# Kernel optimization log

Measured on AMD Instinct MI355X. Metric: run time of the kernel, lower is better.

Reference implementation:

```python
import jax, jax.numpy as jnp
import numpy as np

N = 100000
EPS = 1e-16

def gat_conv(x, edge_index, W, a_src, a_dst, bias, heads, out_c):
    # x: [N, F_in]; W: [F_in, heads*out_c]; a_src/a_dst: [heads, out_c]; bias: [heads*out_c]
    n = x.shape[0]
    loops = jnp.arange(n)
    src = jnp.concatenate([edge_index[0], loops])  # add self loops (PyG default)
    dst = jnp.concatenate([edge_index[1], loops])
    h = (x @ W).reshape(n, heads, out_c)                       # [N,H,C]
    s_src = jnp.sum(h * a_src[None], axis=-1)                  # [N,H]
    s_dst = jnp.sum(h * a_dst[None], axis=-1)                  # [N,H]
    e = jax.nn.leaky_relu(s_src[src] + s_dst[dst], 0.2)        # [E,H]
    m = jax.ops.segment_max(e, dst, num_segments=n)            # [N,H]
    ex = jnp.exp(e - m[dst])
    denom = jax.ops.segment_sum(ex, dst, num_segments=n)       # [N,H]
    alpha = ex / (denom[dst] + EPS)                            # [E,H]
    msg = h[src] * alpha[:, :, None]                           # [E,H,C]
    out = jax.ops.segment_sum(msg, dst, num_segments=n)        # [N,H,C]
    return out.reshape(n, heads * out_c) + bias

def setup_inputs() -> dict:
    key = jax.random.key(0)
    ks = jax.random.split(key, 10)
    num_features, num_classes, H = 512, 10, 8
    E = 3200000
    x = jax.random.normal(ks[0], (N, num_features), dtype=jnp.float32)
    edge_index = jax.random.randint(ks[1], (2, E), 0, N, dtype=jnp.int64)
    g = lambda k, shape, fan: jax.random.normal(k, shape, dtype=jnp.float32) * (1.0 / np.sqrt(fan))
    W1 = g(ks[2], (num_features, H * 8), num_features)
    a_src1 = g(ks[3], (H, 8), 8)
    a_dst1 = g(ks[4], (H, 8), 8)
    b1 = jnp.zeros((H * 8,), dtype=jnp.float32)
    W2 = g(ks[5], (H * 8, H * num_classes), H * 8)
    a_src2 = g(ks[6], (H, num_classes), num_classes)
    a_dst2 = g(ks[7], (H, num_classes), num_classes)
    b2 = jnp.zeros((H * num_classes,), dtype=jnp.float32)
    return {"x": x, "edge_index": edge_index, "W1": W1, "a_src1": a_src1,
            "a_dst1": a_dst1, "b1": b1, "W2": W2, "a_src2": a_src2,
            "a_dst2": a_dst2, "b2": b2}

def reference(x, edge_index, W1, a_src1, a_dst1, b1, W2, a_src2, a_dst2, b2):
    # inference mode: dropout = identity
    h = jax.nn.elu(gat_conv(x, edge_index, W1, a_src1, a_dst1, b1, heads=8, out_c=8))
    out = gat_conv(h, edge_index, W2, a_src2, a_dst2, b2, heads=8, out_c=10)
    return jax.nn.log_softmax(out, axis=1)
```

## Files before the change

### kernel.cpp

```cpp
#include <hip/hip_runtime.h>
#include <math.h>

#define NN 100000
#define NE 3200000
#define FIN 512
#define NH 8
#define C1 8
#define HC1 64
#define C2 10
#define HC2 80

#define EPB 4096
#define NBLK 782
#define NBUK 196
#define SCN (NBUK * NBLK)
#define SCNB 150

typedef unsigned int uint;
typedef unsigned short ushort;
using bf16x8 = __attribute__((ext_vector_type(8))) short;
using f32x4  = __attribute__((ext_vector_type(4))) float;

__device__ float g_h1[NN * HC1];
__device__ float g_hact[NN * HC1];
__device__ float g_h2[NN * HC2];
__device__ uint  g_h1b[NN * 32];
__device__ uint  g_h2b[NN * 40];
__device__ uint  g_w1bt[64 * 256];
__device__ float g_ssrc[NN * NH];
__device__ float g_sdst[NN * NH];
__device__ int   g_off[NN + 1];
__device__ uint  g_pscan[SCN];
__device__ uint  g_bsum2[256];
__device__ uint  g_ebuf[NE];
__device__ int   g_csr[NE];

__device__ __forceinline__ float lrelu(float x) { return fmaxf(x, 0.2f * x); }

__device__ __forceinline__ uint bf16_rne(float x) {
  uint u = __float_as_uint(x);
  u += 0x7fffu + ((u >> 16) & 1u);
  return u >> 16;
}
__device__ __forceinline__ uint packbf2(float lo, float hi) {
  return bf16_rne(lo) | (bf16_rne(hi) << 16);
}
__device__ __forceinline__ float blo(uint v) { return __uint_as_float(v << 16); }
__device__ __forceinline__ float bhi(uint v) { return __uint_as_float(v & 0xffff0000u); }

__global__ __launch_bounds__(256) void p1count_kernel(const int* __restrict__ ei) {
  __shared__ uint cnt[NBUK];
  int tid = threadIdx.x;
  for (int i = tid; i < NBUK; i += 256) cnt[i] = 0;
  __syncthreads();
  const int* dstp = ei + NE;
  int base = blockIdx.x * EPB;
#pragma unroll 4
  for (int k = 0; k < 16; k++) {
    int e = base + k * 256 + tid;
    if (e < NE) atomicAdd(&cnt[dstp[e] >> 9], 1u);
  }
  __syncthreads();
  for (int i = tid; i < NBUK; i += 256) g_pscan[i * NBLK + blockIdx.x] = cnt[i];
}

__global__ __launch_bounds__(1024) void scn_block_kernel() {
  __shared__ uint sd[1024];
  int tid = threadIdx.x;
  int i = blockIdx.x * 1024 + tid;
  uint v = (i < SCN) ? g_pscan[i] : 0;
  sd[tid] = v;
  __syncthreads();
  for (int off = 1; off < 1024; off <<= 1) {
    uint x = (tid >= off) ? sd[tid - off] : 0;
    __syncthreads();
    sd[tid] += x;
    __syncthreads();
  }
  if (i < SCN) g_pscan[i] = sd[tid] - v;
  if (tid == 1023) g_bsum2[blockIdx.x] = sd[1023];
}

__global__ void scn_tops_kernel() {
  __shared__ uint sd[256];
  int tid = threadIdx.x;
  uint v = (tid < SCNB) ? g_bsum2[tid] : 0;
  sd[tid] = v;
  __syncthreads();
  for (int off = 1; off < 256; off <<= 1) {
    uint x = (tid >= off) ? sd[tid - off] : 0;
    __syncthreads();
    sd[tid] += x;
    __syncthreads();
  }
  g_bsum2[tid] = sd[tid] - v;
}

__global__ __launch_bounds__(1024) void scn_add_kernel() {
  int i = blockIdx.x * 1024 + threadIdx.x;
  if (i < SCN) g_pscan[i] += g_bsum2[i >> 10];
}

__global__ __launch_bounds__(256) void p1scatter_kernel(const int* __restrict__ ei) {
  __shared__ uint cur[NBUK];
  int tid = threadIdx.x;
  for (int i = tid; i < NBUK; i += 256) cur[i] = g_pscan[i * NBLK + blockIdx.x];
  __syncthreads();
  const int* srcp = ei;
  const int* dstp = ei + NE;
  int base = blockIdx.x * EPB;
#pragma unroll 4
  for (int k = 0; k < 16; k++) {
    int e = base + k * 256 + tid;
    if (e < NE) {
      int d = dstp[e], s = srcp[e];
      uint pos = atomicAdd(&cur[d >> 9], 1u);
      g_ebuf[pos] = ((uint)(d & 511) << 17) | (uint)s;
    }
  }
}

__global__ __launch_bounds__(1024) void p2build_kernel() {
  __shared__ uint hist[4096];
  __shared__ uint excl[4096];
  __shared__ uint tsum[1024];
  int tid = threadIdx.x;
  int b = blockIdx.x;
  uint bstart = g_pscan[b * NBLK];
  uint bend = (b < NBUK - 1) ? g_pscan[(b + 1) * NBLK] : NE;
  for (int i = tid; i < 4096; i += 1024) hist[i] = 0;
  __syncthreads();
  for (uint j = bstart + tid; j < bend; j += 1024) {
    uint v = g_ebuf[j];
    uint bin = ((v >> 17) << 3) | ((v & 0x1FFFFu) >> 14);
    atomicAdd(&hist[bin], 1u);
  }
  __syncthreads();
  uint h0 = hist[tid * 4 + 0], h1 = hist[tid * 4 + 1];
  uint h2 = hist[tid * 4 + 2], h3 = hist[tid * 4 + 3];
  uint s1 = h0 + h1, s2 = s1 + h2, s3 = s2 + h3;
  tsum[tid] = s3;
  __syncthreads();
  for (int off = 1; off < 1024; off <<= 1) {
    uint x = (tid >= off) ? tsum[tid - off] : 0;
    __syncthreads();
    tsum[tid] += x;
    __syncthreads();
  }
  uint te = tsum[tid] - s3;
  excl[tid * 4 + 0] = te;
  excl[tid * 4 + 1] = te + h0;
  excl[tid * 4 + 2] = te + s1;
  excl[tid * 4 + 3] = te + s2;
  __syncthreads();
  if (tid < 512) {
    int dst = b * 512 + tid;
    if (dst < NN) g_off[dst] = (int)(bstart + excl[tid * 8]);
  }
  if (b == NBUK - 1 && tid == 0) g_off[NN] = NE;
  for (int i = tid; i < 4096; i += 1024) hist[i] = excl[i];
  __syncthreads();
  for (uint j = bstart + tid; j < bend; j += 1024) {
    uint v = g_ebuf[j];
    uint bin = ((v >> 17) << 3) | ((v & 0x1FFFFu) >> 14);
    uint pos = bstart + atomicAdd(&hist[bin], 1u);
    g_csr[pos] = (int)(v & 0x1FFFFu);
  }
}

__global__ __launch_bounds__(256) void w1cast_kernel(const float* __restrict__ W) {
  int idx = blockIdx.x * 256 + threadIdx.x;
  int n = idx & 63, kp = idx >> 6;
  float lo = W[(2 * kp) * HC1 + n];
  float hi = W[(2 * kp + 1) * HC1 + n];
  g_w1bt[n * 256 + kp] = packbf2(lo, hi);
}

__device__ __forceinline__ int sw_idx(int row, int g) {
  return row * 32 + ((g ^ (row & 7)) << 2);
}

__global__ __launch_bounds__(256) void gemm1_kernel(const float* __restrict__ X) {
  __shared__ uint sA[64 * 32];
  __shared__ uint sB[64 * 32];
  int t = threadIdx.x;
  int w = t >> 6, l = t & 63;
  int q = l >> 4, c = l & 15;
  int r0 = blockIdx.x * 64;
  int sr = t >> 2;
  int sc = t & 3;
  int xrow = r0 + sr; if (xrow >= NN) xrow = NN - 1;
  const float* xbase = &X[(long)xrow * FIN + sc * 16];
  const uint* wbase = &g_w1bt[sr * 256 + sc * 8];
  f32x4 acc[4] = {{0.f,0.f,0.f,0.f},{0.f,0.f,0.f,0.f},{0.f,0.f,0.f,0.f},{0.f,0.f,0.f,0.f}};
  for (int k0 = 0; k0 < FIN; k0 += 64) {
    __syncthreads();
    float4 f0 = *(const float4*)&xbase[k0 + 0];
    float4 f1 = *(const float4*)&xbase[k0 + 4];
    float4 f2 = *(const float4*)&xbase[k0 + 8];
    float4 f3 = *(const float4*)&xbase[k0 + 12];
    uint4 a0 = make_uint4(packbf2(f0.x, f0.y), packbf2(f0.z, f0.w),
                          packbf2(f1.x, f1.y), packbf2(f1.z, f1.w));
    uint4 a1 = make_uint4(packbf2(f2.x, f2.y), packbf2(f2.z, f2.w),
                          packbf2(f3.x, f3.y), packbf2(f3.z, f3.w));
    *(uint4*)&sA[sw_idx(sr, sc * 2 + 0)] = a0;
    *(uint4*)&sA[sw_idx(sr, sc * 2 + 1)] = a1;
    uint4 b0 = *(const uint4*)&wbase[(k0 >> 1) + 0];
    uint4 b1 = *(const uint4*)&wbase[(k0 >> 1) + 4];
    *(uint4*)&sB[sw_idx(sr, sc * 2 + 0)] = b0;
    *(uint4*)&sB[sw_idx(sr, sc * 2 + 1)] = b1;
    __syncthreads();
#pragma unroll
    for (int ks = 0; ks < 2; ks++) {
      int g = ks * 4 + q;
      bf16x8 a = *(const bf16x8*)&sA[sw_idx(w * 16 + c, g)];
#pragma unroll
      for (int nt = 0; nt < 4; nt++) {
        bf16x8 b = *(const bf16x8*)&sB[sw_idx(nt * 16 + c, g)];
        acc[nt] = __builtin_amdgcn_mfma_f32_16x16x32_bf16(a, b, acc[nt], 0, 0, 0);
      }
    }
  }
  int orow0 = r0 + w * 16 + q * 4;
#pragma unroll
  for (int nt = 0; nt < 4; nt++) {
#pragma unroll
    for (int r = 0; r < 4; r++) {
      int row = orow0 + r;
      if (row < NN) g_h1[row * HC1 + nt * 16 + c] = acc[nt][r];
    }
  }
}

template <int LAYER>
__global__ __launch_bounds__(256) void s_kernel(const float* __restrict__ a_src,
                                                const float* __restrict__ a_dst) {
  constexpr int C = (LAYER == 1) ? C1 : C2;
  const float* Hm = (LAYER == 1) ? g_h1 : g_h2;
  uint* Hb = (LAYER == 1) ? g_h1b : g_h2b;
  int t = blockIdx.x * 256 + threadIdx.x;
  if (t >= NN * NH) return;
  int h = t & 7;
  const float* row = &Hm[t * C];
  float ss = 0.f, sdd = 0.f;
  float vals[C];
#pragma unroll
  for (int c = 0; c < C; c++) {
    float v = row[c];
    vals[c] = v;
    ss = fmaf(v, a_src[h * C + c], ss);
    sdd = fmaf(v, a_dst[h * C + c], sdd);
  }
  g_ssrc[t] = ss;
  g_sdst[t] = sdd;
#pragma unroll
  for (int j = 0; j < C / 2; j++)
    Hb[t * (C / 2) + j] = packbf2(vals[2 * j], vals[2 * j + 1]);
}

__global__ __launch_bounds__(256) void agg1_kernel(const float* __restrict__ b1) {
  int gw = __builtin_amdgcn_readfirstlane((int)((blockIdx.x * 256 + threadIdx.x) >> 6));
  if (gw >= NN) return;
  int lane = threadIdx.x & 63;
  int h = lane >> 3;
  const ushort* __restrict__ h1u = (const ushort*)g_h1b;
  float sd = g_sdst[gw * NH + h];
  int begin = g_off[gw];
  int cnt = g_off[gw + 1] - begin;
  float acc = 0.f, wsum = 0.f;
  int j = 0;
  for (; j + 4 <= cnt; j += 4) {
    int s0 = __builtin_amdgcn_readfirstlane(g_csr[begin + j + 0]);
    int s1 = __builtin_amdgcn_readfirstlane(g_csr[begin + j + 1]);
    int s2 = __builtin_amdgcn_readfirstlane(g_csr[begin + j + 2]);
    int s3 = __builtin_amdgcn_readfirstlane(g_csr[begin + j + 3]);
    float t0 = g_ssrc[s0 * NH + h];
    float t1 = g_ssrc[s1 * NH + h];
    float t2 = g_ssrc[s2 * NH + h];
    float t3 = g_ssrc[s3 * NH + h];
    uint v0 = h1u[s0 * HC1 + lane];
    uint v1 = h1u[s1 * HC1 + lane];
    uint v2 = h1u[s2 * HC1 + lane];
    uint v3 = h1u[s3 * HC1 + lane];
    float e0 = __expf(lrelu(t0 + sd));
    float e1 = __expf(lrelu(t1 + sd));
    float e2 = __expf(lrelu(t2 + sd));
    float e3 = __expf(lrelu(t3 + sd));
    acc = fmaf(__uint_as_float(v0 << 16), e0, acc);
    acc = fmaf(__uint_as_float(v1 << 16), e1, acc);
    acc = fmaf(__uint_as_float(v2 << 16), e2, acc);
    acc = fmaf(__uint_as_float(v3 << 16), e3, acc);
    wsum += (e0 + e1) + (e2 + e3);
  }
  for (; j < cnt; j++) {
    int s = __builtin_amdgcn_readfirstlane(g_csr[begin + j]);
    float e = __expf(lrelu(g_ssrc[s * NH + h] + sd));
    acc = fmaf(__uint_as_float((uint)h1u[s * HC1 + lane] << 16), e, acc);
    wsum += e;
  }
  float es = __expf(lrelu(g_ssrc[gw * NH + h] + sd));
  acc = fmaf(g_h1[gw * HC1 + lane], es, acc);
  wsum += es;
  float v = acc * (1.f / wsum) + b1[lane];
  g_hact[gw * HC1 + lane] = v > 0.f ? v : __expf(v) - 1.f;
}

__global__ __launch_bounds__(256) void gemm2_kernel(const float* __restrict__ W) {
  __shared__ float sW[64 * HC2 + 64];
  int tid = threadIdx.x;
  for (int i = tid; i < 64 * HC2; i += 256) sW[i] = W[i];
  for (int i = 64 * HC2 + tid; i < 64 * HC2 + 64; i += 256) sW[i] = 0.f;
  __syncthreads();
  int lane = tid & 63;
  int w0 = (blockIdx.x * 256 + tid) >> 6;
  for (int r = w0; r < NN; r += 8192) {
    float v = g_hact[r * HC1 + lane];
    float acc0 = 0.f, acc1 = 0.f;
#pragma unroll
    for (int k = 0; k < 64; k++) {
      float xk = __shfl(v, k);
      acc0 = fmaf(xk, sW[k * HC2 + lane], acc0);
      acc1 = fmaf(xk, sW[k * HC2 + 64 + lane], acc1);
    }
    g_h2[r * HC2 + lane] = acc0;
    if (lane < 16) g_h2[r * HC2 + 64 + lane] = acc1;
  }
}

__global__ __launch_bounds__(256) void agg2_kernel(float* __restrict__ out,
                                                   const float* __restrict__ b2) {
  int gw = __builtin_amdgcn_readfirstlane((int)((blockIdx.x * 256 + threadIdx.x) >> 6));
  if (gw >= NN) return;
  int lane = threadIdx.x & 63;
  int p = lane < 40 ? lane : 39;
  int h = p / 5;
  float sd = g_sdst[gw * NH + h];
  int begin = g_off[gw];
  int cnt = g_off[gw + 1] - begin;
  float acc0 = 0.f, acc1 = 0.f, wsum = 0.f;
  int j = 0;
  for (; j + 4 <= cnt; j += 4) {
    int s0 = __builtin_amdgcn_readfirstlane(g_csr[begin + j + 0]);
    int s1 = __builtin_amdgcn_readfirstlane(g_csr[begin + j + 1]);
    int s2 = __builtin_amdgcn_readfirstlane(g_csr[begin + j + 2]);
    int s3 = __builtin_amdgcn_readfirstlane(g_csr[begin + j + 3]);
    float t0 = g_ssrc[s0 * NH + h];
    float t1 = g_ssrc[s1 * NH + h];
    float t2 = g_ssrc[s2 * NH + h];
    float t3 = g_ssrc[s3 * NH + h];
    uint v0 = g_h2b[s0 * 40 + p];
    uint v1 = g_h2b[s1 * 40 + p];
    uint v2 = g_h2b[s2 * 40 + p];
    uint v3 = g_h2b[s3 * 40 + p];
    float e0 = __expf(lrelu(t0 + sd));
    float e1 = __expf(lrelu(t1 + sd));
    float e2 = __expf(lrelu(t2 + sd));
    float e3 = __expf(lrelu(t3 + sd));
    acc0 = fmaf(blo(v0), e0, acc0); acc1 = fmaf(bhi(v0), e0, acc1);
    acc0 = fmaf(blo(v1), e1, acc0); acc1 = fmaf(bhi(v1), e1, acc1);
    acc0 = fmaf(blo(v2), e2, acc0); acc1 = fmaf(bhi(v2), e2, acc1);
    acc0 = fmaf(blo(v3), e3, acc0); acc1 = fmaf(bhi(v3), e3, acc1);
    wsum += (e0 + e1) + (e2 + e3);
  }
  for (; j < cnt; j++) {
    int s = __builtin_amdgcn_readfirstlane(g_csr[begin + j]);
    float e = __expf(lrelu(g_ssrc[s * NH + h] + sd));
    uint v = g_h2b[s * 40 + p];
    acc0 = fmaf(blo(v), e, acc0); acc1 = fmaf(bhi(v), e, acc1);
    wsum += e;
  }
  float es = __expf(lrelu(g_ssrc[gw * NH + h] + sd));
  acc0 = fmaf(g_h2[gw * HC2 + 2 * p], es, acc0);
  acc1 = fmaf(g_h2[gw * HC2 + 2 * p + 1], es, acc1);
  wsum += es;
  float inv = 1.f / wsum;
  float v0 = acc0 * inv + b2[2 * p];
  float v1 = acc1 * inv + b2[2 * p + 1];
  float mx = fmaxf(v0, v1);
  for (int o = 32; o; o >>= 1) mx = fmaxf(mx, __shfl_xor(mx, o));
  float spart = (lane < 40) ? __expf(v0 - mx) + __expf(v1 - mx) : 0.f;
  for (int o = 32; o; o >>= 1) spart += __shfl_xor(spart, o);
  float lse = mx + __logf(spart);
  if (lane < 40) *(float2*)&out[gw * HC2 + 2 * p] = make_float2(v0 - lse, v1 - lse);
}

extern "C" void kernel_launch(void* const* d_in, const int* in_sizes, int n_in,
                              void* d_out, int out_size, void* d_ws, size_t ws_size,
                              hipStream_t stream) {
  (void)in_sizes; (void)n_in; (void)out_size; (void)d_ws; (void)ws_size;
  const float* x   = (const float*)d_in[0];
  const int*   ei  = (const int*)d_in[1];
  const float* W1  = (const float*)d_in[2];
  const float* as1 = (const float*)d_in[3];
  const float* ad1 = (const float*)d_in[4];
  const float* b1  = (const float*)d_in[5];
  const float* W2  = (const float*)d_in[6];
  const float* as2 = (const float*)d_in[7];
  const float* ad2 = (const float*)d_in[8];
  const float* b2  = (const float*)d_in[9];
  float* out = (float*)d_out;

  p1count_kernel<<<NBLK, 256, 0, stream>>>(ei);
  scn_block_kernel<<<SCNB, 1024, 0, stream>>>();
  scn_tops_kernel<<<1, 256, 0, stream>>>();
  scn_add_kernel<<<SCNB, 1024, 0, stream>>>();
  p1scatter_kernel<<<NBLK, 256, 0, stream>>>(ei);
  p2build_kernel<<<NBUK, 1024, 0, stream>>>();

  w1cast_kernel<<<64, 256, 0, stream>>>(W1);
  gemm1_kernel<<<1563, 256, 0, stream>>>(x);
  s_kernel<1><<<3125, 256, 0, stream>>>(as1, ad1);
  agg1_kernel<<<25000, 256, 0, stream>>>(b1);

  gemm2_kernel<<<2048, 256, 0, stream>>>(W2);
  s_kernel<2><<<3125, 256, 0, stream>>>(as2, ad2);
  agg2_kernel<<<25000, 256, 0, stream>>>(out, b2);
}
```

Before: 794.4 us.

## Aggregate eight nodes per wave in source-range rounds for cache locality

The CSR build now keeps per-node offsets split into eight source-index sub-ranges (g_off8). Each aggregation wave handles eight destination nodes and walks the sub-ranges in rounds, starting at a different round per block (blockIdx & 7) and placing a block-wide barrier after each round. The aim is for concurrently running waves to gather from the same slice of source features at once, so the random gathers hit in L2/MALL instead of DRAM. In exchange it launches fewer waves, holds more per-wave registers, and adds barriers and extra offset loads.

```diff
diff --git a/kernel.cpp b/kernel.cpp
--- a/kernel.cpp
+++ b/kernel.cpp
@@ -29,7 +29,7 @@
 __device__ uint  g_w1bt[64 * 256];
 __device__ float g_ssrc[NN * NH];
 __device__ float g_sdst[NN * NH];
-__device__ int   g_off[NN + 1];
+__device__ int   g_off8[NBUK * 4096];
 __device__ uint  g_pscan[SCN];
 __device__ uint  g_bsum2[256];
 __device__ uint  g_ebuf[NE];
@@ -153,11 +153,8 @@
   excl[tid * 4 + 2] = te + s1;
   excl[tid * 4 + 3] = te + s2;
   __syncthreads();
-  if (tid < 512) {
-    int dst = b * 512 + tid;
-    if (dst < NN) g_off[dst] = (int)(bstart + excl[tid * 8]);
-  }
-  if (b == NBUK - 1 && tid == 0) g_off[NN] = NE;
+  for (int i = tid; i < 4096; i += 1024)
+    g_off8[b * 4096 + i] = (int)(bstart + excl[i]);
   for (int i = tid; i < 4096; i += 1024) hist[i] = excl[i];
   __syncthreads();
   for (uint j = bstart + tid; j < bend; j += 1024) {
@@ -259,50 +256,69 @@
 }
 
 __global__ __launch_bounds__(256) void agg1_kernel(const float* __restrict__ b1) {
-  int gw = __builtin_amdgcn_readfirstlane((int)((blockIdx.x * 256 + threadIdx.x) >> 6));
-  if (gw >= NN) return;
+  int wv = __builtin_amdgcn_readfirstlane((int)((blockIdx.x * 256 + threadIdx.x) >> 6));
+  int n0 = wv * 8;
   int lane = threadIdx.x & 63;
   int h = lane >> 3;
+  int xcd = blockIdx.x & 7;
   const ushort* __restrict__ h1u = (const ushort*)g_h1b;
-  float sd = g_sdst[gw * NH + h];
-  int begin = g_off[gw];
-  int cnt = g_off[gw + 1] - begin;
-  float acc = 0.f, wsum = 0.f;
-  int j = 0;
-  for (; j + 4 <= cnt; j += 4) {
-    int s0 = __builtin_amdgcn_readfirstlane(g_csr[begin + j + 0]);
-    int s1 = __builtin_amdgcn_readfirstlane(g_csr[begin + j + 1]);
-    int s2 = __builtin_amdgcn_readfirstlane(g_csr[begin + j + 2]);
-    int s3 = __builtin_amdgcn_readfirstlane(g_csr[begin + j + 3]);
-    float t0 = g_ssrc[s0 * NH + h];
-    float t1 = g_ssrc[s1 * NH + h];
-    float t2 = g_ssrc[s2 * NH + h];
-    float t3 = g_ssrc[s3 * NH + h];
-    uint v0 = h1u[s0 * HC1 + lane];
-    uint v1 = h1u[s1 * HC1 + lane];
-    uint v2 = h1u[s2 * HC1 + lane];
-    uint v3 = h1u[s3 * HC1 + lane];
-    float e0 = __expf(lrelu(t0 + sd));
-    float e1 = __expf(lrelu(t1 + sd));
-    float e2 = __expf(lrelu(t2 + sd));
-    float e3 = __expf(lrelu(t3 + sd));
-    acc = fmaf(__uint_as_float(v0 << 16), e0, acc);
-    acc = fmaf(__uint_as_float(v1 << 16), e1, acc);
-    acc = fmaf(__uint_as_float(v2 << 16), e2, acc);
-    acc = fmaf(__uint_as_float(v3 << 16), e3, acc);
-    wsum += (e0 + e1) + (e2 + e3);
-  }
-  for (; j < cnt; j++) {
-    int s = __builtin_amdgcn_readfirstlane(g_csr[begin + j]);
-    float e = __expf(lrelu(g_ssrc[s * NH + h] + sd));
-    acc = fmaf(__uint_as_float((uint)h1u[s * HC1 + lane] << 16), e, acc);
-    wsum += e;
-  }
-  float es = __expf(lrelu(g_ssrc[gw * NH + h] + sd));
-  acc = fmaf(g_h1[gw * HC1 + lane], es, acc);
-  wsum += es;
-  float v = acc * (1.f / wsum) + b1[lane];
-  g_hact[gw * HC1 + lane] = v > 0.f ? v : __expf(v) - 1.f;
+  float acc[8], wsum[8], sdv[8];
+#pragma unroll
+  for (int s = 0; s < 8; s++) {
+    acc[s] = 0.f;
+    wsum[s] = 0.f;
+    sdv[s] = g_sdst[(n0 + s) * NH + h];
+  }
+  for (int rr = 0; rr < 8; rr++) {
+    int ra = (rr + xcd) & 7;
+#pragma unroll
+    for (int s = 0; s < 8; s++) {
+      int n = n0 + s;
+      int j  = __builtin_amdgcn_readfirstlane(g_off8[n * 8 + ra]);
+      int j1 = __builtin_amdgcn_readfirstlane(g_off8[n * 8 + ra + 1]);
+      if (j == j1) continue;
+      float sd = sdv[s];
+      for (; j + 4 <= j1; j += 4) {
+        int s0 = __builtin_amdgcn_readfirstlane(g_csr[j + 0]);
+        int s1 = __builtin_amdgcn_readfirstlane(g_csr[j + 1]);
+        int s2 = __builtin_amdgcn_readfirstlane(g_csr[j + 2]);
+        int s3 = __builtin_amdgcn_readfirstlane(g_csr[j + 3]);
+        float t0 = g_ssrc[s0 * NH + h];
+        float t1 = g_ssrc[s1 * NH + h];
+        float t2 = g_ssrc[s2 * NH + h];
+        float t3 = g_ssrc[s3 * NH + h];
+        uint v0 = h1u[s0 * HC1 + lane];
+        uint v1 = h1u[s1 * HC1 + lane];
+        uint v2 = h1u[s2 * HC1 + lane];
+        uint v3 = h1u[s3 * HC1 + lane];
+        float e0 = __expf(lrelu(t0 + sd));
+        float e1 = __expf(lrelu(t1 + sd));
+        float e2 = __expf(lrelu(t2 + sd));
+        float e3 = __expf(lrelu(t3 + sd));
+        acc[s] = fmaf(__uint_as_float(v0 << 16), e0, acc[s]);
+        acc[s] = fmaf(__uint_as_float(v1 << 16), e1, acc[s]);
+        acc[s] = fmaf(__uint_as_float(v2 << 16), e2, acc[s]);
+        acc[s] = fmaf(__uint_as_float(v3 << 16), e3, acc[s]);
+        wsum[s] += (e0 + e1) + (e2 + e3);
+      }
+      for (; j < j1; j++) {
+        int sx = __builtin_amdgcn_readfirstlane(g_csr[j]);
+        float e = __expf(lrelu(g_ssrc[sx * NH + h] + sd));
+        acc[s] = fmaf(__uint_as_float((uint)h1u[sx * HC1 + lane] << 16), e, acc[s]);
+        wsum[s] += e;
+      }
+    }
+    __syncthreads();
+  }
+#pragma unroll
+  for (int s = 0; s < 8; s++) {
+    int n = n0 + s;
+    float es = __expf(lrelu(g_ssrc[n * NH + h] + sdv[s]));
+    float a = fmaf(g_h1[n * HC1 + lane], es, acc[s]);
+    float ws = wsum[s] + es;
+    float v = a * (1.f / ws) + b1[lane];
+    g_hact[n * HC1 + lane] = v > 0.f ? v : __expf(v) - 1.f;
+  }
 }
 
 __global__ __launch_bounds__(256) void gemm2_kernel(const float* __restrict__ W) {
@@ -329,59 +345,79 @@
 
 __global__ __launch_bounds__(256) void agg2_kernel(float* __restrict__ out,
                                                    const float* __restrict__ b2) {
-  int gw = __builtin_amdgcn_readfirstlane((int)((blockIdx.x * 256 + threadIdx.x) >> 6));
-  if (gw >= NN) return;
+  int wv = __builtin_amdgcn_readfirstlane((int)((blockIdx.x * 256 + threadIdx.x) >> 6));
+  int n0 = wv * 8;
   int lane = threadIdx.x & 63;
   int p = lane < 40 ? lane : 39;
   int h = p / 5;
-  float sd = g_sdst[gw * NH + h];
-  int begin = g_off[gw];
-  int cnt = g_off[gw + 1] - begin;
-  float acc0 = 0.f, acc1 = 0.f, wsum = 0.f;
-  int j = 0;
-  for (; j + 4 <= cnt; j += 4) {
-    int s0 = __builtin_amdgcn_readfirstlane(g_csr[begin + j + 0]);
-    int s1 = __builtin_amdgcn_readfirstlane(g_csr[begin + j + 1]);
-    int s2 = __builtin_amdgcn_readfirstlane(g_csr[begin + j + 2]);
-    int s3 = __builtin_amdgcn_readfirstlane(g_csr[begin + j + 3]);
-    float t0 = g_ssrc[s0 * NH + h];
-    float t1 = g_ssrc[s1 * NH + h];
-    float t2 = g_ssrc[s2 * NH + h];
-    float t3 = g_ssrc[s3 * NH + h];
-    uint v0 = g_h2b[s0 * 40 + p];
-    uint v1 = g_h2b[s1 * 40 + p];
-    uint v2 = g_h2b[s2 * 40 + p];
-    uint v3 = g_h2b[s3 * 40 + p];
-    float e0 = __expf(lrelu(t0 + sd));
-    float e1 = __expf(lrelu(t1 + sd));
-    float e2 = __expf(lrelu(t2 + sd));
-    float e3 = __expf(lrelu(t3 + sd));
-    acc0 = fmaf(blo(v0), e0, acc0); acc1 = fmaf(bhi(v0), e0, acc1);
-    acc0 = fmaf(blo(v1), e1, acc0); acc1 = fmaf(bhi(v1), e1, acc1);
-    acc0 = fmaf(blo(v2), e2, acc0); acc1 = fmaf(bhi(v2), e2, acc1);
-    acc0 = fmaf(blo(v3), e3, acc0); acc1 = fmaf(bhi(v3), e3, acc1);
-    wsum += (e0 + e1) + (e2 + e3);
-  }
-  for (; j < cnt; j++) {
-    int s = __builtin_amdgcn_readfirstlane(g_csr[begin + j]);
-    float e = __expf(lrelu(g_ssrc[s * NH + h] + sd));
-    uint v = g_h2b[s * 40 + p];
-    acc0 = fmaf(blo(v), e, acc0); acc1 = fmaf(bhi(v), e, acc1);
-    wsum += e;
-  }
-  float es = __expf(lrelu(g_ssrc[gw * NH + h] + sd));
-  acc0 = fmaf(g_h2[gw * HC2 + 2 * p], es, acc0);
-  acc1 = fmaf(g_h2[gw * HC2 + 2 * p + 1], es, acc1);
-  wsum += es;
-  float inv = 1.f / wsum;
-  float v0 = acc0 * inv + b2[2 * p];
-  float v1 = acc1 * inv + b2[2 * p + 1];
-  float mx = fmaxf(v0, v1);
-  for (int o = 32; o; o >>= 1) mx = fmaxf(mx, __shfl_xor(mx, o));
-  float spart = (lane < 40) ? __expf(v0 - mx) + __expf(v1 - mx) : 0.f;
-  for (int o = 32; o; o >>= 1) spart += __shfl_xor(spart, o);
-  float lse = mx + __logf(spart);
-  if (lane < 40) *(float2*)&out[gw * HC2 + 2 * p] = make_float2(v0 - lse, v1 - lse);
+  int xcd = blockIdx.x & 7;
+  float acc0[8], acc1[8], wsum[8], sdv[8];
+#pragma unroll
+  for (int s = 0; s < 8; s++) {
+    acc0[s] = 0.f;
+    acc1[s] = 0.f;
+    wsum[s] = 0.f;
+    sdv[s] = g_sdst[(n0 + s) * NH + h];
+  }
+  for (int rr = 0; rr < 8; rr++) {
+    int ra = (rr + xcd) & 7;
+#pragma unroll
+    for (int s = 0; s < 8; s++) {
+      int n = n0 + s;
+      int j  = __builtin_amdgcn_readfirstlane(g_off8[n * 8 + ra]);
+      int j1 = __builtin_amdgcn_readfirstlane(g_off8[n * 8 + ra + 1]);
+      if (j == j1) continue;
+      float sd = sdv[s];
+      for (; j + 4 <= j1; j += 4) {
+        int s0 = __builtin_amdgcn_readfirstlane(g_csr[j + 0]);
+        int s1 = __builtin_amdgcn_readfirstlane(g_csr[j + 1]);
+        int s2 = __builtin_amdgcn_readfirstlane(g_csr[j + 2]);
+        int s3 = __builtin_amdgcn_readfirstlane(g_csr[j + 3]);
+        float t0 = g_ssrc[s0 * NH + h];
+        float t1 = g_ssrc[s1 * NH + h];
+        float t2 = g_ssrc[s2 * NH + h];
+        float t3 = g_ssrc[s3 * NH + h];
+        uint v0 = g_h2b[s0 * 40 + p];
+        uint v1 = g_h2b[s1 * 40 + p];
+        uint v2 = g_h2b[s2 * 40 + p];
+        uint v3 = g_h2b[s3 * 40 + p];
+        float e0 = __expf(lrelu(t0 + sd));
+        float e1 = __expf(lrelu(t1 + sd));
+        float e2 = __expf(lrelu(t2 + sd));
+        float e3 = __expf(lrelu(t3 + sd));
+        acc0[s] = fmaf(blo(v0), e0, acc0[s]); acc1[s] = fmaf(bhi(v0), e0, acc1[s]);
+        acc0[s] = fmaf(blo(v1), e1, acc0[s]); acc1[s] = fmaf(bhi(v1), e1, acc1[s]);
+        acc0[s] = fmaf(blo(v2), e2, acc0[s]); acc1[s] = fmaf(bhi(v2), e2, acc1[s]);
+        acc0[s] = fmaf(blo(v3), e3, acc0[s]); acc1[s] = fmaf(bhi(v3), e3, acc1[s]);
+        wsum[s] += (e0 + e1) + (e2 + e3);
+      }
+      for (; j < j1; j++) {
+        int sx = __builtin_amdgcn_readfirstlane(g_csr[j]);
+        float e = __expf(lrelu(g_ssrc[sx * NH + h] + sd));
+        uint v = g_h2b[sx * 40 + p];
+        acc0[s] = fmaf(blo(v), e, acc0[s]); acc1[s] = fmaf(bhi(v), e, acc1[s]);
+        wsum[s] += e;
+      }
+    }
+    __syncthreads();
+  }
+#pragma unroll
+  for (int s = 0; s < 8; s++) {
+    int n = n0 + s;
+    float es = __expf(lrelu(g_ssrc[n * NH + h] + sdv[s]));
+    float a0 = fmaf(g_h2[n * HC2 + 2 * p], es, acc0[s]);
+    float a1 = fmaf(g_h2[n * HC2 + 2 * p + 1], es, acc1[s]);
+    float ws = wsum[s] + es;
+    float inv = 1.f / ws;
+    float v0 = a0 * inv + b2[2 * p];
+    float v1 = a1 * inv + b2[2 * p + 1];
+    float mx = fmaxf(v0, v1);
+    for (int o = 32; o; o >>= 1) mx = fmaxf(mx, __shfl_xor(mx, o));
+    float spart = (lane < 40) ? __expf(v0 - mx) + __expf(v1 - mx) : 0.f;
+    for (int o = 32; o; o >>= 1) spart += __shfl_xor(spart, o);
+    float lse = mx + __logf(spart);
+    if (lane < 40) *(float2*)&out[n * HC2 + 2 * p] = make_float2(v0 - lse, v1 - lse);
+  }
 }
 
 extern "C" void kernel_launch(void* const* d_in, const int* in_sizes, int n_in,
@@ -410,9 +446,9 @@
   w1cast_kernel<<<64, 256, 0, stream>>>(W1);
   gemm1_kernel<<<1563, 256, 0, stream>>>(x);
   s_kernel<1><<<3125, 256, 0, stream>>>(as1, ad1);
-  agg1_kernel<<<25000, 256, 0, stream>>>(b1);
+  agg1_kernel<<<3125, 256, 0, stream>>>(b1);
 
   gemm2_kernel<<<2048, 256, 0, stream>>>(W2);
   s_kernel<2><<<3125, 256, 0, stream>>>(as2, ad2);
-  agg2_kernel<<<25000, 256, 0, stream>>>(out, b2);
-}
+  agg2_kernel<<<3125, 256, 0, stream>>>(out, b2);
+}
```

Result: slower. 890.8 us (+12.1%).

## Process four edges per wavefront concurrently in GAT aggregation kernels

Applied to the files above, without the earlier changes.

Both aggregation kernels now split each 64-lane wavefront into four 16-lane groups. Each group handles a different neighbor edge, and each lane accumulates 4-5 channels from wider vector loads. Partial sums are combined with cross-group shuffles at the end. To support this, layer-2 bf16 features are repacked per head-half: four channels go in a uint2 and the fifth in a separate ushort region. The goal is more memory-level parallelism per gathered row and fewer wasted lanes, in exchange for extra reductions and masked lanes on the remainder loop.

```diff
diff --git a/kernel.cpp b/kernel.cpp
--- a/kernel.cpp
+++ b/kernel.cpp
@@ -20,6 +20,8 @@
 typedef unsigned short ushort;
 using bf16x8 = __attribute__((ext_vector_type(8))) short;
 using f32x4  = __attribute__((ext_vector_type(4))) float;
+
+#define RFL(x) __builtin_amdgcn_readfirstlane((int)(x))
 
 __device__ float g_h1[NN * HC1];
 __device__ float g_hact[NN * HC1];
@@ -237,7 +239,6 @@
                                                 const float* __restrict__ a_dst) {
   constexpr int C = (LAYER == 1) ? C1 : C2;
   const float* Hm = (LAYER == 1) ? g_h1 : g_h2;
-  uint* Hb = (LAYER == 1) ? g_h1b : g_h2b;
   int t = blockIdx.x * 256 + threadIdx.x;
   if (t >= NN * NH) return;
   int h = t & 7;
@@ -253,56 +254,81 @@
   }
   g_ssrc[t] = ss;
   g_sdst[t] = sdd;
-#pragma unroll
-  for (int j = 0; j < C / 2; j++)
-    Hb[t * (C / 2) + j] = packbf2(vals[2 * j], vals[2 * j + 1]);
+  if constexpr (LAYER == 1) {
+#pragma unroll
+    for (int j = 0; j < 4; j++)
+      g_h1b[t * 4 + j] = packbf2(vals[2 * j], vals[2 * j + 1]);
+  } else {
+    int n = t >> 3;
+#pragma unroll
+    for (int b = 0; b < 2; b++) {
+      int il = 2 * h + b;
+      g_h2b[n * 40 + 2 * il + 0] = packbf2(vals[5 * b + 0], vals[5 * b + 1]);
+      g_h2b[n * 40 + 2 * il + 1] = packbf2(vals[5 * b + 2], vals[5 * b + 3]);
+      ((ushort*)&g_h2b[n * 40 + 32])[il] = (ushort)bf16_rne(vals[5 * b + 4]);
+    }
+  }
 }
 
 __global__ __launch_bounds__(256) void agg1_kernel(const float* __restrict__ b1) {
-  int gw = __builtin_amdgcn_readfirstlane((int)((blockIdx.x * 256 + threadIdx.x) >> 6));
+  int gw = RFL((blockIdx.x * 256 + threadIdx.x) >> 6);
   if (gw >= NN) return;
   int lane = threadIdx.x & 63;
-  int h = lane >> 3;
-  const ushort* __restrict__ h1u = (const ushort*)g_h1b;
-  float sd = g_sdst[gw * NH + h];
-  int begin = g_off[gw];
-  int cnt = g_off[gw + 1] - begin;
-  float acc = 0.f, wsum = 0.f;
-  int j = 0;
-  for (; j + 4 <= cnt; j += 4) {
-    int s0 = __builtin_amdgcn_readfirstlane(g_csr[begin + j + 0]);
-    int s1 = __builtin_amdgcn_readfirstlane(g_csr[begin + j + 1]);
-    int s2 = __builtin_amdgcn_readfirstlane(g_csr[begin + j + 2]);
-    int s3 = __builtin_amdgcn_readfirstlane(g_csr[begin + j + 3]);
-    float t0 = g_ssrc[s0 * NH + h];
-    float t1 = g_ssrc[s1 * NH + h];
-    float t2 = g_ssrc[s2 * NH + h];
-    float t3 = g_ssrc[s3 * NH + h];
-    uint v0 = h1u[s0 * HC1 + lane];
-    uint v1 = h1u[s1 * HC1 + lane];
-    uint v2 = h1u[s2 * HC1 + lane];
-    uint v3 = h1u[s3 * HC1 + lane];
-    float e0 = __expf(lrelu(t0 + sd));
-    float e1 = __expf(lrelu(t1 + sd));
-    float e2 = __expf(lrelu(t2 + sd));
-    float e3 = __expf(lrelu(t3 + sd));
-    acc = fmaf(__uint_as_float(v0 << 16), e0, acc);
-    acc = fmaf(__uint_as_float(v1 << 16), e1, acc);
-    acc = fmaf(__uint_as_float(v2 << 16), e2, acc);
-    acc = fmaf(__uint_as_float(v3 << 16), e3, acc);
-    wsum += (e0 + e1) + (e2 + e3);
-  }
-  for (; j < cnt; j++) {
-    int s = __builtin_amdgcn_readfirstlane(g_csr[begin + j]);
-    float e = __expf(lrelu(g_ssrc[s * NH + h] + sd));
-    acc = fmaf(__uint_as_float((uint)h1u[s * HC1 + lane] << 16), e, acc);
-    wsum += e;
-  }
-  float es = __expf(lrelu(g_ssrc[gw * NH + h] + sd));
-  acc = fmaf(g_h1[gw * HC1 + lane], es, acc);
-  wsum += es;
-  float v = acc * (1.f / wsum) + b1[lane];
-  g_hact[gw * HC1 + lane] = v > 0.f ? v : __expf(v) - 1.f;
+  int sl = lane >> 4, il = lane & 15;
+  int hh = il >> 1;
+  bool sl1 = (sl & 1) != 0, sl2 = (sl & 2) != 0;
+  float sdl = g_sdst[gw * NH + hh];
+  float4 bb = *(const float4*)&b1[4 * il];
+  int j = g_off[gw];
+  int jend = g_off[gw + 1];
+  if (jend < j) jend = j;
+  float a0A=0.f,a1A=0.f,a2A=0.f,a3A=0.f,wA=0.f;
+  float a0B=0.f,a1B=0.f,a2B=0.f,a3B=0.f,wB=0.f;
+#define G1(A0,A1,A2,A3,WW,J) {                                       \
+    int s0 = RFL(g_csr[(J)+0]), s1 = RFL(g_csr[(J)+1]);              \
+    int s2 = RFL(g_csr[(J)+2]), s3 = RFL(g_csr[(J)+3]);              \
+    int ssx = sl2 ? (sl1 ? s3 : s2) : (sl1 ? s1 : s0);               \
+    float tt = g_ssrc[ssx * NH + hh];                                \
+    uint2 va = *(const uint2*)&g_h1b[ssx * 32 + 2 * il];             \
+    float e = __expf(lrelu(tt + sdl));                               \
+    A0 = fmaf(blo(va.x), e, A0); A1 = fmaf(bhi(va.x), e, A1);        \
+    A2 = fmaf(blo(va.y), e, A2); A3 = fmaf(bhi(va.y), e, A3);        \
+    WW += e; }
+  for (; j + 8 <= jend; j += 8) {
+    G1(a0A,a1A,a2A,a3A,wA,j)
+    G1(a0B,a1B,a2B,a3B,wB,j+4)
+  }
+  if (j + 4 <= jend) { G1(a0A,a1A,a2A,a3A,wA,j); j += 4; }
+#undef G1
+  for (; j < jend; j++) {
+    int s0 = RFL(g_csr[j]);
+    float tt = g_ssrc[s0 * NH + hh];
+    uint2 va = *(const uint2*)&g_h1b[s0 * 32 + 2 * il];
+    float e = (sl == 0) ? __expf(lrelu(tt + sdl)) : 0.f;
+    a0B = fmaf(blo(va.x), e, a0B); a1B = fmaf(bhi(va.x), e, a1B);
+    a2B = fmaf(blo(va.y), e, a2B); a3B = fmaf(bhi(va.y), e, a3B);
+    wB += e;
+  }
+  float a0 = a0A + a0B, a1 = a1A + a1B, a2 = a2A + a2B, a3 = a3A + a3B;
+  float w = wA + wB;
+  a0 += __shfl_xor(a0, 16); a0 += __shfl_xor(a0, 32);
+  a1 += __shfl_xor(a1, 16); a1 += __shfl_xor(a1, 32);
+  a2 += __shfl_xor(a2, 16); a2 += __shfl_xor(a2, 32);
+  a3 += __shfl_xor(a3, 16); a3 += __shfl_xor(a3, 32);
+  w  += __shfl_xor(w, 16);  w  += __shfl_xor(w, 32);
+  float es = __expf(lrelu(g_ssrc[gw * NH + hh] + sdl));
+  float4 hv = *(const float4*)&g_h1[gw * HC1 + 4 * il];
+  a0 = fmaf(hv.x, es, a0); a1 = fmaf(hv.y, es, a1);
+  a2 = fmaf(hv.z, es, a2); a3 = fmaf(hv.w, es, a3);
+  w += es;
+  float inv = 1.f / w;
+  float v0 = a0 * inv + bb.x, v1 = a1 * inv + bb.y;
+  float v2 = a2 * inv + bb.z, v3 = a3 * inv + bb.w;
+  v0 = v0 > 0.f ? v0 : __expf(v0) - 1.f;
+  v1 = v1 > 0.f ? v1 : __expf(v1) - 1.f;
+  v2 = v2 > 0.f ? v2 : __expf(v2) - 1.f;
+  v3 = v3 > 0.f ? v3 : __expf(v3) - 1.f;
+  if (sl == 0) *(float4*)&g_hact[gw * HC1 + 4 * il] = make_float4(v0, v1, v2, v3);
 }
 
 __global__ __launch_bounds__(256) void gemm2_kernel(const float* __restrict__ W) {
@@ -329,59 +355,78 @@
 
 __global__ __launch_bounds__(256) void agg2_kernel(float* __restrict__ out,
                                                    const float* __restrict__ b2) {
-  int gw = __builtin_amdgcn_readfirstlane((int)((blockIdx.x * 256 + threadIdx.x) >> 6));
+  int gw = RFL((blockIdx.x * 256 + threadIdx.x) >> 6);
   if (gw >= NN) return;
   int lane = threadIdx.x & 63;
-  int p = lane < 40 ? lane : 39;
-  int h = p / 5;
-  float sd = g_sdst[gw * NH + h];
-  int begin = g_off[gw];
-  int cnt = g_off[gw + 1] - begin;
-  float acc0 = 0.f, acc1 = 0.f, wsum = 0.f;
-  int j = 0;
-  for (; j + 4 <= cnt; j += 4) {
-    int s0 = __builtin_amdgcn_readfirstlane(g_csr[begin + j + 0]);
-    int s1 = __builtin_amdgcn_readfirstlane(g_csr[begin + j + 1]);
-    int s2 = __builtin_amdgcn_readfirstlane(g_csr[begin + j + 2]);
-    int s3 = __builtin_amdgcn_readfirstlane(g_csr[begin + j + 3]);
-    float t0 = g_ssrc[s0 * NH + h];
-    float t1 = g_ssrc[s1 * NH + h];
-    float t2 = g_ssrc[s2 * NH + h];
-    float t3 = g_ssrc[s3 * NH + h];
-    uint v0 = g_h2b[s0 * 40 + p];
-    uint v1 = g_h2b[s1 * 40 + p];
-    uint v2 = g_h2b[s2 * 40 + p];
-    uint v3 = g_h2b[s3 * 40 + p];
-    float e0 = __expf(lrelu(t0 + sd));
-    float e1 = __expf(lrelu(t1 + sd));
-    float e2 = __expf(lrelu(t2 + sd));
-    float e3 = __expf(lrelu(t3 + sd));
-    acc0 = fmaf(blo(v0), e0, acc0); acc1 = fmaf(bhi(v0), e0, acc1);
-    acc0 = fmaf(blo(v1), e1, acc0); acc1 = fmaf(bhi(v1), e1, acc1);
-    acc0 = fmaf(blo(v2), e2, acc0); acc1 = fmaf(bhi(v2), e2, acc1);
-    acc0 = fmaf(blo(v3), e3, acc0); acc1 = fmaf(bhi(v3), e3, acc1);
-    wsum += (e0 + e1) + (e2 + e3);
-  }
-  for (; j < cnt; j++) {
-    int s = __builtin_amdgcn_readfirstlane(g_csr[begin + j]);
-    float e = __expf(lrelu(g_ssrc[s * NH + h] + sd));
-    uint v = g_h2b[s * 40 + p];
-    acc0 = fmaf(blo(v), e, acc0); acc1 = fmaf(bhi(v), e, acc1);
-    wsum += e;
-  }
-  float es = __expf(lrelu(g_ssrc[gw * NH + h] + sd));
-  acc0 = fmaf(g_h2[gw * HC2 + 2 * p], es, acc0);
-  acc1 = fmaf(g_h2[gw * HC2 + 2 * p + 1], es, acc1);
-  wsum += es;
-  float inv = 1.f / wsum;
-  float v0 = acc0 * inv + b2[2 * p];
-  float v1 = acc1 * inv + b2[2 * p + 1];
-  float mx = fmaxf(v0, v1);
-  for (int o = 32; o; o >>= 1) mx = fmaxf(mx, __shfl_xor(mx, o));
-  float spart = (lane < 40) ? __expf(v0 - mx) + __expf(v1 - mx) : 0.f;
-  for (int o = 32; o; o >>= 1) spart += __shfl_xor(spart, o);
-  float lse = mx + __logf(spart);
-  if (lane < 40) *(float2*)&out[gw * HC2 + 2 * p] = make_float2(v0 - lse, v1 - lse);
+  int sl = lane >> 4, il = lane & 15;
+  int hh = il >> 1, bq = il & 1;
+  int c0 = 10 * hh + 5 * bq;
+  bool sl1 = (sl & 1) != 0, sl2 = (sl & 2) != 0;
+  float sdl = g_sdst[gw * NH + hh];
+  float bb0 = b2[c0 + 0], bb1 = b2[c0 + 1], bb2 = b2[c0 + 2];
+  float bb3 = b2[c0 + 3], bb4 = b2[c0 + 4];
+  int j = g_off[gw];
+  int jend = g_off[gw + 1];
+  if (jend < j) jend = j;
+  float a0A=0.f,a1A=0.f,a2A=0.f,a3A=0.f,a4A=0.f,wA=0.f;
+  float a0B=0.f,a1B=0.f,a2B=0.f,a3B=0.f,a4B=0.f,wB=0.f;
+#define G2(A0,A1,A2,A3,A4,WW,J) {                                    \
+    int s0 = RFL(g_csr[(J)+0]), s1 = RFL(g_csr[(J)+1]);              \
+    int s2 = RFL(g_csr[(J)+2]), s3 = RFL(g_csr[(J)+3]);              \
+    int ssx = sl2 ? (sl1 ? s3 : s2) : (sl1 ? s1 : s0);               \
+    float tt = g_ssrc[ssx * NH + hh];                                \
+    uint2 va = *(const uint2*)&g_h2b[ssx * 40 + 2 * il];             \
+    uint vb = ((const ushort*)&g_h2b[ssx * 40 + 32])[il];            \
+    float e = __expf(lrelu(tt + sdl));                               \
+    A0 = fmaf(blo(va.x), e, A0); A1 = fmaf(bhi(va.x), e, A1);        \
+    A2 = fmaf(blo(va.y), e, A2); A3 = fmaf(bhi(va.y), e, A3);        \
+    A4 = fmaf(__uint_as_float(vb << 16), e, A4);                     \
+    WW += e; }
+  for (; j + 8 <= jend; j += 8) {
+    G2(a0A,a1A,a2A,a3A,a4A,wA,j)
+    G2(a0B,a1B,a2B,a3B,a4B,wB,j+4)
+  }
+  if (j + 4 <= jend) { G2(a0A,a1A,a2A,a3A,a4A,wA,j); j += 4; }
+#undef G2
+  for (; j < jend; j++) {
+    int s0 = RFL(g_csr[j]);
+    float tt = g_ssrc[s0 * NH + hh];
+    uint2 va = *(const uint2*)&g_h2b[s0 * 40 + 2 * il];
+    uint vb = ((const ushort*)&g_h2b[s0 * 40 + 32])[il];
+    float e = (sl == 0) ? __expf(lrelu(tt + sdl)) : 0.f;
+    a0B = fmaf(blo(va.x), e, a0B); a1B = fmaf(bhi(va.x), e, a1B);
+    a2B = fmaf(blo(va.y), e, a2B); a3B = fmaf(bhi(va.y), e, a3B);
+    a4B = fmaf(__uint_as_float(vb << 16), e, a4B);
+    wB += e;
+  }
+  float a0 = a0A + a0B, a1 = a1A + a1B, a2 = a2A + a2B;
+  float a3 = a3A + a3B, a4 = a4A + a4B, w = wA + wB;
+  a0 += __shfl_xor(a0, 16); a0 += __shfl_xor(a0, 32);
+  a1 += __shfl_xor(a1, 16); a1 += __shfl_xor(a1, 32);
+  a2 += __shfl_xor(a2, 16); a2 += __shfl_xor(a2, 32);
+  a3 += __shfl_xor(a3, 16); a3 += __shfl_xor(a3, 32);
+  a4 += __shfl_xor(a4, 16); a4 += __shfl_xor(a4, 32);
+  w  += __shfl_xor(w, 16);  w  += __shfl_xor(w, 32);
+  float es = __expf(lrelu(g_ssrc[gw * NH + hh] + sdl));
+  const float* h2row = &g_h2[gw * HC2 + c0];
+  a0 = fmaf(h2row[0], es, a0); a1 = fmaf(h2row[1], es, a1);
+  a2 = fmaf(h2row[2], es, a2); a3 = fmaf(h2row[3], es, a3);
+  a4 = fmaf(h2row[4], es, a4);
+  w += es;
+  float inv = 1.f / w;
+  float v0 = a0 * inv + bb0, v1 = a1 * inv + bb1, v2 = a2 * inv + bb2;
+  float v3 = a3 * inv + bb3, v4 = a4 * inv + bb4;
+  float mx = fmaxf(fmaxf(fmaxf(v0, v1), fmaxf(v2, v3)), v4);
+  for (int o = 1; o < 16; o <<= 1) mx = fmaxf(mx, __shfl_xor(mx, o));
+  float sp = __expf(v0 - mx) + __expf(v1 - mx) + __expf(v2 - mx) +
+             __expf(v3 - mx) + __expf(v4 - mx);
+  for (int o = 1; o < 16; o <<= 1) sp += __shfl_xor(sp, o);
+  float lse = mx + __logf(sp);
+  if (sl == 0) {
+    float* op = &out[gw * HC2 + c0];
+    op[0] = v0 - lse; op[1] = v1 - lse; op[2] = v2 - lse;
+    op[3] = v3 - lse; op[4] = v4 - lse;
+  }
 }
 
 extern "C" void kernel_launch(void* const* d_in, const int* in_sizes, int n_in,
```

After: 785.5 us. About the same (-1.1%).
